# Performance work log

Hardware: AMD Instinct MI355X
Metric: run time of the kernel (lower is better)

The kernel has to match this reference:

```python
import jax, jax.numpy as jnp
import numpy as np

B, T, N, C = 64, 256, 21, 3
HID, HEADS, HDIM, DOUT = 128, 4, 32, 256
CDIM, DMODEL = 64, 256
DINNER, DSTATE, DCONV, DTRANK, L = 512, 16, 4, 16, 4
NSIGNS, NHS, NLOC, NMOV, NORI = 2000, 40, 20, 20, 8
TEMP = 0.07

def _ln(x, w):
    mu = x.mean(-1, keepdims=True)
    var = ((x - mu) ** 2).mean(-1, keepdims=True)
    return (x - mu) / jnp.sqrt(var + 1e-5) * w

def _silu(x):
    return x * jax.nn.sigmoid(x)

def _causal_conv(u, w, b):  # u:(B,T,D), depthwise causal conv, w:(D,K)
    K = w.shape[1]
    up = jnp.pad(u, ((0, 0), (K - 1, 0), (0, 0)))
    y = sum(up[:, k:k + u.shape[1], :] * w[:, k] for k in range(K))
    return y + b

def _scan(u, dt, Bm, Cm, A, Dp):  # selective SSM scan; u,dt:(B,T,Di), Bm,Cm:(B,T,Ds)
    def step(h, xs):
        dt_t, b_t, c_t, u_t = xs
        dA = jnp.exp(dt_t[..., None] * A)                       # (B,Di,Ds)
        dBu = dt_t[..., None] * b_t[:, None, :] * u_t[..., None]
        h = dA * h + dBu
        y = jnp.einsum('bds,bs->bd', h, c_t)
        return h, y
    h0 = jnp.zeros((u.shape[0], A.shape[0], A.shape[1]), u.dtype)
    xs = (dt.swapaxes(0, 1), Bm.swapaxes(0, 1), Cm.swapaxes(0, 1), u.swapaxes(0, 1))
    _, ys = jax.lax.scan(step, h0, xs)
    return ys.swapaxes(0, 1) + u * Dp

def _cos_logits(f, p):
    fn = f / (jnp.linalg.norm(f, axis=-1, keepdims=True) + 1e-8)
    pn = p / (jnp.linalg.norm(p, axis=-1, keepdims=True) + 1e-8)
    return fn @ pn.T / TEMP

def _forward(x, agan_w_in, agan_b_in, agan_w_gat, agan_a_src, agan_a_dst,
             agan_w_out, agan_b_out, pdm_w, pdm_b, pdm_w_fuse, pdm_b_fuse,
             ssm_ln_w, ssm_in_proj, ssm_conv_w, ssm_conv_b, ssm_x_proj,
             ssm_dt_w, ssm_dt_b, ssm_A_log, ssm_D, ssm_out_proj,
             hpc_w_sign, hpc_b_sign, sign_protos, proto_hs, proto_loc,
             proto_mov, proto_ori):
    # ---- AGAN: multi-head graph attention over N landmarks per frame ----
    h0 = jax.nn.relu(x @ agan_w_in + agan_b_in)                  # (B,T,N,HID)
    h = jnp.einsum('btni,hio->btnho', h0, agan_w_gat)            # (B,T,N,H,O)
    src = jnp.einsum('btnho,ho->btnh', h, agan_a_src)
    dst = jnp.einsum('btnho,ho->btnh', h, agan_a_dst)
    e = jax.nn.leaky_relu(src[:, :, :, None, :] + dst[:, :, None, :, :], 0.2)  # (B,T,Ni,Nj,H)
    alpha = jax.nn.softmax(e, axis=3)
    agg = jnp.einsum('btijh,btjho->btiho', alpha, h).reshape(h0.shape)
    feat = jax.nn.relu(h0 + agg)
    spatial = (feat @ agan_w_out + agan_b_out).mean(axis=2)      # (B,T,DOUT)
    # ---- PDM: 4 phonological component projections + fusion ----
    comps = jax.nn.relu(jnp.einsum('btd,kdc->btkc', spatial, pdm_w) + pdm_b)  # (B,T,4,CDIM)
    fused = comps.reshape(B, T, 4 * CDIM) @ pdm_w_fuse + pdm_b_fuse           # (B,T,DMODEL)
    # ---- BiSSM: bidirectional selective SSM layers with residuals ----
    xx = fused
    for l in range(L):
        xn = _ln(xx, ssm_ln_w[l])
        ysum = 0.0
        for d in range(2):
            u_in = xn if d == 0 else xn[:, ::-1]
            xz = u_in @ ssm_in_proj[l, d]
            u, z = xz[..., :DINNER], xz[..., DINNER:]
            u = _silu(_causal_conv(u, ssm_conv_w[l, d], ssm_conv_b[l, d]))
            xdbl = u @ ssm_x_proj[l, d]
            dt = jax.nn.softplus(xdbl[..., :DTRANK] @ ssm_dt_w[l, d] + ssm_dt_b[l, d])
            Bm = xdbl[..., DTRANK:DTRANK + DSTATE]
            Cm = xdbl[..., DTRANK + DSTATE:]
            A = -jnp.exp(ssm_A_log[l, d])
            y = _scan(u, dt, Bm, Cm, A, ssm_D[l, d]) * _silu(z)
            y = y @ ssm_out_proj[l, d]
            ysum = ysum + (y if d == 0 else y[:, ::-1])
        xx = xx + ysum
    temporal = xx
    # ---- HPC: prototype classifier ----
    emb = temporal.mean(axis=1) @ hpc_w_sign + hpc_b_sign        # (B,DMODEL)
    logits = _cos_logits(emb, sign_protos)                       # (B,NSIGNS)
    pooled_c = comps.mean(axis=1)                                # (B,4,CDIM)
    sims = tuple(_cos_logits(pooled_c[:, k], p)
                 for k, p in enumerate((proto_hs, proto_loc, proto_mov, proto_ori)))
    return (logits, emb) + sims

def setup_inputs():
    key = jax.random.key(0)
    ks = iter(jax.random.split(key, 40))
    def rn(shape, scale):
        return jax.random.normal(next(ks), shape, jnp.float32) * scale
    inp = {}
    inp['x'] = rn((B, T, N, C), 1.0)
    inp['agan_w_in'] = rn((C, HID), C ** -0.5)
    inp['agan_b_in'] = jnp.zeros((HID,), jnp.float32)
    inp['agan_w_gat'] = rn((HEADS, HID, HDIM), HID ** -0.5)
    inp['agan_a_src'] = rn((HEADS, HDIM), 0.1)
    inp['agan_a_dst'] = rn((HEADS, HDIM), 0.1)
    inp['agan_w_out'] = rn((HID, DOUT), HID ** -0.5)
    inp['agan_b_out'] = jnp.zeros((DOUT,), jnp.float32)
    inp['pdm_w'] = rn((4, DOUT, CDIM), DOUT ** -0.5)
    inp['pdm_b'] = jnp.zeros((4, CDIM), jnp.float32)
    inp['pdm_w_fuse'] = rn((4 * CDIM, DMODEL), (4 * CDIM) ** -0.5)
    inp['pdm_b_fuse'] = jnp.zeros((DMODEL,), jnp.float32)
    inp['ssm_ln_w'] = jnp.ones((L, DMODEL), jnp.float32)
    inp['ssm_in_proj'] = rn((L, 2, DMODEL, 2 * DINNER), DMODEL ** -0.5)
    inp['ssm_conv_w'] = rn((L, 2, DINNER, DCONV), DCONV ** -0.5)
    inp['ssm_conv_b'] = jnp.zeros((L, 2, DINNER), jnp.float32)
    inp['ssm_x_proj'] = rn((L, 2, DINNER, DTRANK + 2 * DSTATE), DINNER ** -0.5)
    inp['ssm_dt_w'] = rn((L, 2, DTRANK, DINNER), DTRANK ** -0.5)
    inp['ssm_dt_b'] = jnp.full((L, 2, DINNER), -4.6, jnp.float32)  # softplus ~ 0.01
    a = jnp.log(jnp.tile(jnp.arange(1, DSTATE + 1, dtype=jnp.float32)[None, :], (DINNER, 1)))
    inp['ssm_A_log'] = jnp.tile(a[None, None], (L, 2, 1, 1))
    inp['ssm_D'] = jnp.ones((L, 2, DINNER), jnp.float32)
    inp['ssm_out_proj'] = rn((L, 2, DINNER, DMODEL), DINNER ** -0.5)
    inp['hpc_w_sign'] = rn((DMODEL, DMODEL), DMODEL ** -0.5)
    inp['hpc_b_sign'] = jnp.zeros((DMODEL,), jnp.float32)
    inp['sign_protos'] = rn((NSIGNS, DMODEL), 1.0)
    inp['proto_hs'] = rn((NHS, CDIM), 1.0)
    inp['proto_loc'] = rn((NLOC, CDIM), 1.0)
    inp['proto_mov'] = rn((NMOV, CDIM), 1.0)
    inp['proto_ori'] = rn((NORI, CDIM), 1.0)
    return inp

def reference(x, agan_w_in, agan_b_in, agan_w_gat, agan_a_src, agan_a_dst,
              agan_w_out, agan_b_out, pdm_w, pdm_b, pdm_w_fuse, pdm_b_fuse,
              ssm_ln_w, ssm_in_proj, ssm_conv_w, ssm_conv_b, ssm_x_proj,
              ssm_dt_w, ssm_dt_b, ssm_A_log, ssm_D, ssm_out_proj,
              hpc_w_sign, hpc_b_sign, sign_protos, proto_hs, proto_loc,
              proto_mov, proto_ori):
    return _forward(x, agan_w_in, agan_b_in, agan_w_gat, agan_a_src, agan_a_dst,
                    agan_w_out, agan_b_out, pdm_w, pdm_b, pdm_w_fuse, pdm_b_fuse,
                    ssm_ln_w, ssm_in_proj, ssm_conv_w, ssm_conv_b, ssm_x_proj,
                    ssm_dt_w, ssm_dt_b, ssm_A_log, ssm_D, ssm_out_proj,
                    hpc_w_sign, hpc_b_sign, sign_protos, proto_hs, proto_loc,
                    proto_mov, proto_ori)
```

## Files before the change

kernel.cpp:

```cpp
#include <hip/hip_runtime.h>
#include <hip/hip_bf16.h>
#include <math.h>

#define BB 64
#define TT 256
#define NNODE 21
#define HID 128
#define DMODEL 256
#define DINNER 512
#define NSIGNS 2000
#define BTT (BB*TT)

typedef unsigned short u16;
typedef unsigned int u32;
typedef __attribute__((ext_vector_type(8))) short short8;
typedef __attribute__((ext_vector_type(4))) float f32x4;

template<int V> struct IC { static constexpr int v = V; };

__device__ __forceinline__ float siluf(float x){ return x/(1.f+expf(-x)); }
__device__ __forceinline__ u16 f2bf(float x){ __hip_bfloat16 h = __float2bfloat16(x); return *(u16*)&h; }
__device__ __forceinline__ u32 pk2bf(float a, float b){
  float2 f2; f2.x = a; f2.y = b;
  __hip_bfloat162 h2 = __float22bfloat162_rn(f2);
  return *(u32*)&h2;
}
__device__ __forceinline__ float bf2f(u16 u){ return __uint_as_float(((u32)u)<<16); }
__device__ __forceinline__ void gload16(const u16* g, u16* l){
  __builtin_amdgcn_global_load_lds((const __attribute__((address_space(1))) void*)g,
                                   (__attribute__((address_space(3))) void*)l, 16, 0, 0);
}

__global__ __launch_bounds__(256) void transpose_w_kernel(
    const float* __restrict__ in_proj, const float* __restrict__ out_proj,
    const float* __restrict__ x_proj, const float* __restrict__ w_out,
    const float* __restrict__ pdm_w, const float* __restrict__ w_fuse,
    const float* __restrict__ w_gat, u16* __restrict__ dst)
{
  __shared__ short tl[64*66];
  int bx = blockIdx.x, tid = threadIdx.x;
  const float* S = nullptr; size_t soff = 0; int lds = 0, Nsrc = 0;
  size_t doff = 0; int ldd = 0, Nout = 0;
  int tn = 0, tk = 0;
  bool zero = false;
  if (bx < 512) {
    int j = bx >> 5, tt = bx & 31;
    int l = j >> 2, d = j & 1, zh = (j >> 1) & 1;
    tn = tt >> 2; tk = tt & 3;
    S = in_proj; soff = ((size_t)(l*2+d)*256)*1024 + zh*512; lds = 1024; Nsrc = 512;
    doff = (size_t)l*524288 + (size_t)(zh*1024 + d*512)*256; ldd = 256; Nout = 512;
  } else if (bx < 768) {
    int j = (bx-512) >> 5, tt = (bx-512) & 31;
    int l = j >> 1, d = j & 1;
    tn = tt >> 3; tk = tt & 7;
    S = out_proj; soff = (size_t)(l*2+d)*512*256; lds = 256; Nsrc = 256;
    doff = 2097152 + (size_t)l*262144 + d*512; ldd = 1024; Nout = 256;
  } else if (bx < 896) {
    int j = (bx-768) >> 3, tt = (bx-768) & 7;
    int l = j >> 2, sub = j & 3;
    tn = 0; tk = tt;
    if (sub < 2) {
      int d = sub;
      S = x_proj; soff = (size_t)(l*2+d)*512*48; lds = 48; Nsrc = 48;
      doff = 3145728 + (size_t)l*131072 + (size_t)(d*64)*1024 + d*512; ldd = 1024; Nout = 64;
    } else {
      int d = sub-2; zero = true;
      doff = 3145728 + (size_t)l*131072 + (size_t)(d*64)*1024 + (1-d)*512; ldd = 1024; Nout = 64;
    }
  } else if (bx < 904) {
    int tt = bx-896; tn = tt>>1; tk = tt&1;
    S = w_out; soff = 0; lds = 256; Nsrc = 256;
    doff = 3670016; ldd = 128; Nout = 256;
  } else if (bx < 920) {
    int j = (bx-904)>>2, tt = (bx-904)&3;
    tn = 0; tk = tt;
    S = pdm_w; soff = (size_t)j*16384; lds = 64; Nsrc = 64;
    doff = 3702784 + (size_t)j*16384; ldd = 256; Nout = 64;
  } else if (bx < 936) {
    int tt = bx-920; tn = tt>>2; tk = tt&3;
    S = w_fuse; soff = 0; lds = 256; Nsrc = 256;
    doff = 3768320; ldd = 256; Nout = 256;
  } else {
    int j = (bx-936)>>1, tt = (bx-936)&1;
    tn = 0; tk = tt;
    S = w_gat; soff = (size_t)j*4096; lds = 32; Nsrc = 32;
    doff = 3833856 + (size_t)j*4096; ldd = 128; Nout = 32;
  }
  int n0 = tn*64, k0 = tk*64;
  if (!zero) {
    #pragma unroll
    for (int i=0;i<16;++i){
      int kk = i*4 + (tid>>6), nn = tid&63;
      float v = (n0+nn < Nsrc) ? S[soff + (size_t)(k0+kk)*lds + n0+nn] : 0.f;
      tl[nn*66+kk] = (short)f2bf(v);
    }
    __syncthreads();
    #pragma unroll
    for (int i=0;i<16;++i){
      int nn = i*4 + (tid>>6), kk = tid&63;
      if (n0+nn < Nout) dst[doff + (size_t)(n0+nn)*ldd + k0+kk] = (u16)tl[nn*66+kk];
    }
  } else {
    #pragma unroll
    for (int i=0;i<16;++i){
      int nn = i*4 + (tid>>6), kk = tid&63;
      if (n0+nn < Nout) dst[doff + (size_t)(n0+nn)*ldd + k0+kk] = 0;
    }
  }
}

__global__ __launch_bounds__(256) void agan_kernel(
    const float* __restrict__ x, const float* __restrict__ w_in, const float* __restrict__ b_in,
    const u16* __restrict__ bpt, const float* __restrict__ a_src, const float* __restrict__ a_dst,
    u16* __restrict__ fsum_out)
{
  int bt = blockIdx.x;
  int tid = threadIdx.x;
  int lane = tid & 63, wid = tid >> 6;
  int lr = lane & 15, lq = lane >> 4;
  __shared__ float xv[NNODE][4];
  __shared__ __align__(16) short sh0[32*136];
  __shared__ __align__(16) short hmT[128*40];
  __shared__ __align__(16) short alb[4*32*40];
  __shared__ float sd[2][NNODE][4];
  __shared__ float sm[4][NNODE];
  short8 bp[4][2];
  #pragma unroll
  for (int ks=0;ks<4;++ks)
    #pragma unroll
    for (int ct=0;ct<2;++ct)
      bp[ks][ct] = *(const short8*)(bpt + (size_t)(wid*32+ct*16+lr)*128 + ks*32 + lq*8);
  int ii = tid & 127, nn0 = tid >> 7;
  float w0 = w_in[ii], w1 = w_in[128+ii], w2 = w_in[256+ii], bi = b_in[ii];
  if (tid < NNODE*3) xv[tid/3][tid%3] = x[(size_t)bt*63 + tid];
  __syncthreads();
  #pragma unroll
  for (int n = 0; n < 32; n += 2) {
    int nr = n + nn0;
    float v = 0.f;
    if (nr < NNODE)
      v = fmaxf(bi + xv[nr][0]*w0 + xv[nr][1]*w1 + xv[nr][2]*w2, 0.f);
    sh0[nr*136 + ii] = (short)f2bf(v);
  }
  __syncthreads();
  {
    f32x4 g00={},g01={},g10={},g11={};
    #pragma unroll
    for (int ks=0;ks<4;++ks){
      short8 a0 = *(const short8*)&sh0[(lr   )*136 + ks*32 + lq*8];
      short8 a1 = *(const short8*)&sh0[(16+lr)*136 + ks*32 + lq*8];
      g00 = __builtin_amdgcn_mfma_f32_16x16x32_bf16(a0, bp[ks][0], g00, 0,0,0);
      g01 = __builtin_amdgcn_mfma_f32_16x16x32_bf16(a0, bp[ks][1], g01, 0,0,0);
      g10 = __builtin_amdgcn_mfma_f32_16x16x32_bf16(a1, bp[ks][0], g10, 0,0,0);
      g11 = __builtin_amdgcn_mfma_f32_16x16x32_bf16(a1, bp[ks][1], g11, 0,0,0);
    }
    f32x4 gg[2][2] = {{g00,g01},{g10,g11}};
    #pragma unroll
    for (int mt=0;mt<2;++mt)
      #pragma unroll
      for (int ct=0;ct<2;++ct){
        int col = wid*32 + ct*16 + lr;
        int row0 = mt*16 + lq*4;
        u32 wv0 = pk2bf(gg[mt][ct][0], gg[mt][ct][1]);
        u32 wv1 = pk2bf(gg[mt][ct][2], gg[mt][ct][3]);
        *(uint2*)&hmT[col*40 + row0] = make_uint2(wv0,wv1);
      }
  }
  __syncthreads();
  if (tid < 168) {
    int which = tid >= 84;
    int r = tid - which*84;
    int n = r >> 2, h = r & 3;
    const float* av = (which ? a_dst : a_src) + h*32;
    float s = 0.f;
    #pragma unroll
    for (int o=0;o<32;++o){ int oo=(o+tid)&31; s += bf2f((u16)hmT[(h*32+oo)*40 + n])*av[oo]; }
    sd[which][n][h] = s;
  }
  __syncthreads();
  if (tid < 84) {
    int i = tid >> 2, h = tid & 3;
    float sv = sd[0][i][h], m = -1e30f;
    #pragma unroll
    for (int j=0;j<NNODE;++j){
      float e = sv + sd[1][j][h];
      e = e>=0.f ? e : 0.2f*e;
      m = fmaxf(m,e);
    }
    sm[h][i] = m;
  }
  __syncthreads();
  for (int idx = tid; idx < 84*32; idx += 256) {
    int j = idx & 31, ih = idx >> 5;
    int i = ih >> 2, h = ih & 3;
    float m = sm[h][i];
    float ex = 0.f;
    if (j < NNODE){
      float e = sd[0][i][h] + sd[1][j][h];
      e = e>=0.f ? e : 0.2f*e;
      ex = __expf(e - m);
    }
    alb[(h*32+i)*40 + j] = (short)f2bf(ex);
    float s = ex;
    #pragma unroll
    for (int off=1; off<32; off<<=1) s += __shfl_xor(s, off);
    if (j == 0) sm[h][i] = 1.f/s;
  }
  __syncthreads();
  {
    int h = wid;
    short8 a0 = *(const short8*)&alb[(h*32 + lr     )*40 + lq*8];
    short8 a1 = *(const short8*)&alb[(h*32 + 16 + lr)*40 + lq*8];
    short8 b0 = *(const short8*)&hmT[(h*32 + lr     )*40 + lq*8];
    short8 b1 = *(const short8*)&hmT[(h*32 + 16 + lr)*40 + lq*8];
    f32x4 c00={},c01={},c10={},c11={};
    c00 = __builtin_amdgcn_mfma_f32_16x16x32_bf16(a0,b0,c00,0,0,0);
    c01 = __builtin_amdgcn_mfma_f32_16x16x32_bf16(a0,b1,c01,0,0,0);
    c10 = __builtin_amdgcn_mfma_f32_16x16x32_bf16(a1,b0,c10,0,0,0);
    c11 = __builtin_amdgcn_mfma_f32_16x16x32_bf16(a1,b1,c11,0,0,0);
    f32x4 cc[2][2] = {{c00,c01},{c10,c11}};
    #pragma unroll
    for (int ct=0; ct<2; ++ct){
      int col = h*32 + ct*16 + lr;
      float s = 0.f;
      #pragma unroll
      for (int mt=0; mt<2; ++mt)
        #pragma unroll
        for (int r=0;r<4;++r){
          int n = mt*16 + lq*4 + r;
          if (n < NNODE)
            s += fmaxf(bf2f((u16)sh0[n*136+col]) + cc[mt][ct][r]*sm[h][n], 0.f);
        }
      s += __shfl_xor(s, 16);
      s += __shfl_xor(s, 32);
      if (lq == 0) fsum_out[(size_t)bt*128 + col] = f2bf(s*(1.f/21.f));
    }
  }
}

template<int ACC, int BIAS, int RELU, int SM>
__global__ __launch_bounds__(256) void gemm_bf16_kernel(
    const u16* __restrict__ A, const u16* __restrict__ BT, const float* __restrict__ bias,
    float* __restrict__ C, u16* __restrict__ C2,
    int M, int N, int K, int lda)
{
  __shared__ __align__(16) short Asl[8192];
  __shared__ __align__(16) short Bsl[8192];
  int tid = threadIdx.x;
  int lane = tid & 63, wid = tid >> 6;
  int wm = wid >> 1, wn = wid & 1;
  int row0 = blockIdx.y*128, col0 = blockIdx.x*128;
  const u16* Ab = A  + (size_t)row0*lda;
  const u16* Bb = BT + (size_t)col0*K;
  f32x4 acc[4][4] = {};
  int lrow = lane & 15, lk = (lane>>4)*8;
  for (int k0 = 0; k0 < K; k0 += 64) {
    #pragma unroll
    for (int is=0; is<4; ++is){
      int li = is*256 + tid;
      int row = li >> 3;
      int c8  = (li & 7) ^ (row & 7);
      gload16(Ab + (size_t)row*lda + k0 + c8*8, (u16*)Asl + ((is<<8)+(wid<<6))*8);
      gload16(Bb + (size_t)row*K   + k0 + c8*8, (u16*)Bsl + ((is<<8)+(wid<<6))*8);
    }
    __syncthreads();
    #pragma unroll
    for (int ksub=0; ksub<2; ++ksub){
      int slot = (ksub*32 + lk) >> 3;
      short8 a[4], b[4];
      #pragma unroll
      for (int i=0;i<4;++i){ int rr=wm*64+i*16+lrow; a[i]=*(const short8*)&Asl[rr*64+((slot^(rr&7))<<3)]; }
      #pragma unroll
      for (int j=0;j<4;++j){ int rr=wn*64+j*16+lrow; b[j]=*(const short8*)&Bsl[rr*64+((slot^(rr&7))<<3)]; }
      #pragma unroll
      for (int i=0;i<4;++i)
        #pragma unroll
        for (int j=0;j<4;++j)
          acc[i][j] = __builtin_amdgcn_mfma_f32_16x16x32_bf16(a[i], b[j], acc[i][j], 0, 0, 0);
    }
    __syncthreads();
  }
  #pragma unroll
  for (int i=0;i<4;++i) {
    int row = row0 + wm*64 + i*16 + (lane>>4)*4;
    #pragma unroll
    for (int j=0;j<4;++j) {
      int col = col0 + wn*64 + j*16 + (lane&15);
      if (col < N) {
        float bv = BIAS ? bias[col] : 0.f;
        #pragma unroll
        for (int r=0;r<4;++r) {
          float v = acc[i][j][r] + bv;
          if (RELU) v = fmaxf(v, 0.f);
          size_t o = (size_t)(row+r)*N + col;
          if (ACC)           C[o] += v;
          else if (SM == 0)  C[o]  = v;
          else               C2[o] = f2bf(v);
        }
      }
    }
  }
}

template<int ACC, int BIAS, int RELU, int SM, int POOL>
__global__ __launch_bounds__(256) void gemm_bm64_kernel(
    const u16* __restrict__ A, const u16* __restrict__ BT, const float* __restrict__ bias,
    float* __restrict__ C, u16* __restrict__ C2, float* __restrict__ pool,
    int M, int N, int K, int lda)
{
  __shared__ __align__(16) short Asl[4096];
  __shared__ __align__(16) short Bsl[8192];
  int tid = threadIdx.x;
  int lane = tid & 63, wid = tid >> 6;
  int wm = wid >> 1, wn = wid & 1;
  int row0 = blockIdx.y*64, col0 = blockIdx.x*128;
  const u16* Ab = A  + (size_t)row0*lda;
  const u16* Bb = BT + (size_t)col0*K;
  f32x4 acc[2][4] = {};
  int lrow = lane & 15, lq = lane >> 4, lk = lq*8;
  for (int k0 = 0; k0 < K; k0 += 64) {
    #pragma unroll
    for (int is=0; is<2; ++is){
      int li = is*256 + tid;
      int row = li >> 3;
      int c8  = (li & 7) ^ (row & 7);
      gload16(Ab + (size_t)row*lda + k0 + c8*8, (u16*)Asl + ((is<<8)+(wid<<6))*8);
    }
    #pragma unroll
    for (int is=0; is<4; ++is){
      int li = is*256 + tid;
      int row = li >> 3;
      int c8  = (li & 7) ^ (row & 7);
      gload16(Bb + (size_t)row*K + k0 + c8*8, (u16*)Bsl + ((is<<8)+(wid<<6))*8);
    }
    __syncthreads();
    #pragma unroll
    for (int ksub=0; ksub<2; ++ksub){
      int slot = (ksub*32 + lk) >> 3;
      short8 a[2], b[4];
      #pragma unroll
      for (int i=0;i<2;++i){ int rr=wm*32+i*16+lrow; a[i]=*(const short8*)&Asl[rr*64+((slot^(rr&7))<<3)]; }
      #pragma unroll
      for (int j=0;j<4;++j){ int rr=wn*64+j*16+lrow; b[j]=*(const short8*)&Bsl[rr*64+((slot^(rr&7))<<3)]; }
      #pragma unroll
      for (int i=0;i<2;++i)
        #pragma unroll
        for (int j=0;j<4;++j)
          acc[i][j] = __builtin_amdgcn_mfma_f32_16x16x32_bf16(a[i], b[j], acc[i][j], 0, 0, 0);
    }
    __syncthreads();
  }
  float colsum[4] = {0.f,0.f,0.f,0.f};
  #pragma unroll
  for (int i=0;i<2;++i) {
    int row = row0 + wm*32 + i*16 + lq*4;
    #pragma unroll
    for (int j=0;j<4;++j) {
      int col = col0 + wn*64 + j*16 + lrow;
      if (col < N) {
        float bv = BIAS ? bias[col] : 0.f;
        #pragma unroll
        for (int r=0;r<4;++r) {
          float v = acc[i][j][r] + bv;
          if (RELU) v = fmaxf(v, 0.f);
          size_t o = (size_t)(row+r)*N + col;
          if (ACC)           C[o] += v;
          else if (SM == 0)  C[o]  = v;
          else               C2[o] = f2bf(v);
          if (POOL) colsum[j] += v;
        }
      }
    }
  }
  if (POOL) {
    float* red = (float*)Asl;
    #pragma unroll
    for (int j=0;j<4;++j) red[tid*4+j] = colsum[j];
    __syncthreads();
    if (tid < 128) {
      int wn_ = tid >> 6, j_ = (tid >> 4) & 3, l15 = tid & 15;
      float s = 0.f;
      #pragma unroll
      for (int wm_=0;wm_<2;++wm_)
        #pragma unroll
        for (int g=0;g<4;++g)
          s += red[(((wm_*2+wn_)*64) + g*16 + l15)*4 + j_];
      pool[(size_t)blockIdx.y*256 + blockIdx.x*128 + tid] = s * (1.f/256.f);
    }
  }
}

__global__ __launch_bounds__(256) void gemm_n64_kernel(
    const u16* __restrict__ A, const u16* __restrict__ BT,
    float* __restrict__ C, int N, int K, int lda)
{
  __shared__ __align__(16) short Asl[4096];
  __shared__ __align__(16) short Bsl[4096];
  int tid = threadIdx.x;
  int lane = tid & 63, wid = tid >> 6;
  int lrow = lane & 15, lq = lane >> 4, lk = lq*8;
  int row0 = blockIdx.y*64, col0 = blockIdx.x*64;
  const u16* Ab = A  + (size_t)row0*lda;
  const u16* Bb = BT + (size_t)col0*K;
  f32x4 acc[4] = {};
  for (int k0 = 0; k0 < K; k0 += 64) {
    #pragma unroll
    for (int is=0; is<2; ++is){
      int li = is*256 + tid;
      int row = li >> 3;
      int c8  = (li & 7) ^ (row & 7);
      gload16(Ab + (size_t)row*lda + k0 + c8*8, (u16*)Asl + ((is<<8)+(wid<<6))*8);
      gload16(Bb + (size_t)row*K   + k0 + c8*8, (u16*)Bsl + ((is<<8)+(wid<<6))*8);
    }
    __syncthreads();
    #pragma unroll
    for (int ksub=0; ksub<2; ++ksub){
      int slot = (ksub*32 + lk) >> 3;
      int arr = wid*16 + lrow;
      short8 av = *(const short8*)&Asl[arr*64 + ((slot^(arr&7))<<3)];
      #pragma unroll
      for (int j=0;j<4;++j){
        int brr = j*16 + lrow;
        short8 bv = *(const short8*)&Bsl[brr*64 + ((slot^(brr&7))<<3)];
        acc[j] = __builtin_amdgcn_mfma_f32_16x16x32_bf16(av, bv, acc[j], 0, 0, 0);
      }
    }
    __syncthreads();
  }
  #pragma unroll
  for (int j=0;j<4;++j){
    int col = col0 + j*16 + lrow;
    #pragma unroll
    for (int r=0;r<4;++r){
      int row = row0 + wid*16 + lq*4 + r;
      C[(size_t)row*N + col] = acc[j][r];
    }
  }
}

__global__ __launch_bounds__(256) void ln_kernel(const float* __restrict__ x,
    const float* __restrict__ w, u16* __restrict__ o)
{
  int row = blockIdx.x*4 + (threadIdx.x>>6);
  int lane = threadIdx.x & 63;
  float4 v = *(const float4*)(x + (size_t)row*DMODEL + lane*4);
  float s = v.x+v.y+v.z+v.w;
  #pragma unroll
  for (int off=32;off>=1;off>>=1) s += __shfl_xor(s, off);
  float mu = s * (1.f/256.f);
  float d0=v.x-mu, d1=v.y-mu, d2=v.z-mu, d3=v.w-mu;
  float q = d0*d0+d1*d1+d2*d2+d3*d3;
  #pragma unroll
  for (int off=32;off>=1;off>>=1) q += __shfl_xor(q, off);
  float inv = 1.f/sqrtf(q*(1.f/256.f) + 1e-5f);
  float4 wv = *(const float4*)(w + lane*4);
  uint2 pk; pk.x = pk2bf(d0*inv*wv.x, d1*inv*wv.y); pk.y = pk2bf(d2*inv*wv.z, d3*inv*wv.w);
  *(uint2*)(o + (size_t)row*DMODEL + lane*4) = pk;
}

__global__ __launch_bounds__(256) void conv_kernel(const u16* __restrict__ xz,
    const float* __restrict__ cw, const float* __restrict__ cb,
    u16* __restrict__ ucv)
{
  int idx = blockIdx.x*256 + threadIdx.x;
  int du8 = idx & 127, dir = du8 >> 6, d8 = (du8 & 63) << 3;
  int bt = idx >> 7, t = bt & 255;
  const u16* up = xz + (size_t)(bt - t)*2048 + dir*512 + d8;
  float w[8][4];
  #pragma unroll
  for (int j=0;j<8;++j){
    float4 wv = *(const float4*)(cw + (size_t)dir*2048 + (d8+j)*4);
    w[j][0]=wv.x; w[j][1]=wv.y; w[j][2]=wv.z; w[j][3]=wv.w;
  }
  float s[8];
  float4 cb0 = *(const float4*)(cb + dir*512 + d8);
  float4 cb1 = *(const float4*)(cb + dir*512 + d8 + 4);
  s[0]=cb0.x; s[1]=cb0.y; s[2]=cb0.z; s[3]=cb0.w;
  s[4]=cb1.x; s[5]=cb1.y; s[6]=cb1.z; s[7]=cb1.w;
  if (dir == 0) {
    #pragma unroll
    for (int k=0;k<4;++k){
      int tk = t-3+k;
      if (tk >= 0){
        short8 uv = *(const short8*)(up + (size_t)tk*2048);
        #pragma unroll
        for (int j=0;j<8;++j) s[j] += w[j][k]*bf2f((u16)uv[j]);
      }
    }
  } else {
    #pragma unroll
    for (int kk=0;kk<4;++kk){
      int tk = t+kk;
      if (tk < TT){
        short8 uv = *(const short8*)(up + (size_t)tk*2048);
        #pragma unroll
        for (int j=0;j<8;++j) s[j] += w[j][3-kk]*bf2f((u16)uv[j]);
      }
    }
  }
  short8 o;
  #pragma unroll
  for (int j=0;j<8;++j) o[j] = (short)f2bf(siluf(s[j]));
  *(short8*)(ucv + (size_t)bt*1024 + dir*512 + d8) = o;
}

template<int FINAL>
__global__ __launch_bounds__(256) void scan_phase_kernel(
    const u16* __restrict__ ucv, const float* __restrict__ xd, const u16* __restrict__ xz,
    const float* __restrict__ dtw, const float* __restrict__ dtb,
    const float* __restrict__ alog, const float* __restrict__ dvec,
    const u16* __restrict__ hend_r, const float* __restrict__ sdt_r,
    float* __restrict__ sdt_w, u16* __restrict__ hend_w,
    u16* __restrict__ yout)
{
  int b = blockIdx.x, c = blockIdx.y, gz = blockIdx.z;
  int d = gz >> 1;
  int tid = threadIdx.x;
  int dd = ((gz & 1) << 8) + tid;
  float wdt[16], Av[16], h[16];
  #pragma unroll
  for (int s=0;s<16;++s){
    wdt[s] = dtw[d*8192 + s*512 + dd];
    Av[s]  = -__expf(alog[d*8192 + dd*16 + s]);
    h[s]   = 0.f;
  }
  float bdt = dtb[d*512 + dd];
  bool powok = true;
  #pragma unroll
  for (int s=0;s<16;++s) powok = powok && (fabsf(Av[s] + (float)(s+1)) < 1e-5f*(float)(s+1));
  __shared__ float sxd[32][48];
  for (int i = tid; i < 1536; i += 256){
    int q = i/48, r = i - q*48;
    int p = (c<<5)+q, t = d ? 255-p : p;
    sxd[q][r] = xd[((size_t)b*TT + t)*128 + d*64 + r];
  }
  if (FINAL) {
    for (int cp=0; cp<c; ++cp){
      size_t cbase = (((size_t)b*8+cp)*2+d)*512 + dd;
      float S = sdt_r[cbase];
      short8 h0v = *(const short8*)(hend_r + cbase*16);
      short8 h1v = *(const short8*)(hend_r + cbase*16 + 8);
      #pragma unroll
      for (int s=0;s<8;++s)  h[s]   = fmaf(__expf(Av[s]*S),   h[s],   bf2f((u16)h0v[s]));
      #pragma unroll
      for (int s=0;s<8;++s)  h[s+8] = fmaf(__expf(Av[s+8]*S), h[s+8], bf2f((u16)h1v[s]));
    }
  }
  __syncthreads();
  float S = 0.f;
  float Dv = FINAL ? dvec[d*512 + dd] : 0.f;
  const u16* ub = ucv + d*512 + dd;
  const u16* zb = xz + 1024 + d*512 + dd;
  u16* yb = yout + d*512 + dd;
  auto qloop = [&](auto icpow){
    constexpr int POW = decltype(icpow)::v;
    #pragma unroll 4
    for (int q=0;q<32;++q) {
      int p = (c<<5)+q, t = d ? 255-p : p;
      size_t row = (size_t)b*TT + t;
      float uc = bf2f(ub[row*1024]);
      float zc = FINAL ? bf2f(zb[row*2048]) : 0.f;
      const float* sr = sxd[q];
      float p0=0.f,p1=0.f,p2=0.f,p3=0.f;
      #pragma unroll
      for (int r=0;r<16;r+=4){
        p0 = fmaf(sr[r+0],wdt[r+0],p0);
        p1 = fmaf(sr[r+1],wdt[r+1],p1);
        p2 = fmaf(sr[r+2],wdt[r+2],p2);
        p3 = fmaf(sr[r+3],wdt[r+3],p3);
      }
      float dtp = bdt + ((p0+p1)+(p2+p3));
      float dt = fmaxf(dtp,0.f) + __logf(1.f + __expf(-fabsf(dtp)));
      float dtu = dt*uc;
      if (!FINAL) S += dt;
      float y0=0.f, y1=0.f;
      if (POW) {
        float rr = __expf(-dt);
        float pw = rr;
        #pragma unroll
        for (int s=0;s<16;++s){
          h[s] = fmaf(pw, h[s], dtu*sr[16+s]);
          if (FINAL) y0 = fmaf(h[s], sr[32+s], y0);
          pw *= rr;
        }
      } else {
        #pragma unroll
        for (int s=0;s<16;s+=2){
          float dA0 = __expf(dt*Av[s]);
          float dA1 = __expf(dt*Av[s+1]);
          h[s]   = fmaf(dA0, h[s],   dtu*sr[16+s]);
          h[s+1] = fmaf(dA1, h[s+1], dtu*sr[16+s+1]);
          if (FINAL){ y0 = fmaf(h[s],sr[32+s],y0); y1 = fmaf(h[s+1],sr[32+s+1],y1); }
        }
      }
      if (FINAL){
        float yv = (y0+y1) + uc*Dv;
        float sg = zc / (1.f + __expf(-zc));
        yb[row*2048] = f2bf(yv*sg);
      }
    }
  };
  if (powok) qloop(IC<1>{}); else qloop(IC<0>{});
  if (!FINAL){
    size_t co = (((size_t)b*8+c)*2+d)*512 + dd;
    sdt_w[co] = S;
    short8 o0, o1;
    #pragma unroll
    for (int s=0;s<8;++s){ o0[s] = (short)f2bf(h[s]); o1[s] = (short)f2bf(h[s+8]); }
    *(short8*)(hend_w + co*16)     = o0;
    *(short8*)(hend_w + co*16 + 8) = o1;
  }
}

__global__ __launch_bounds__(256) void emb_kernel(const float* __restrict__ xx,
    const float* __restrict__ wsgn, const float* __restrict__ bsgn,
    float* __restrict__ embw, float* __restrict__ out)
{
  int b = blockIdx.x, tid = threadIdx.x;
  __shared__ float mt[256];
  float s0=0.f,s1=0.f,s2=0.f,s3=0.f;
  for (int t=0;t<TT;t+=4){
    s0 += xx[((size_t)b*TT+t  )*DMODEL + tid];
    s1 += xx[((size_t)b*TT+t+1)*DMODEL + tid];
    s2 += xx[((size_t)b*TT+t+2)*DMODEL + tid];
    s3 += xx[((size_t)b*TT+t+3)*DMODEL + tid];
  }
  mt[tid] = (s0+s1+s2+s3)*(1.f/256.f);
  __syncthreads();
  float acc = bsgn[tid];
  for (int i=0;i<DMODEL;++i) acc += mt[i]*wsgn[i*DMODEL + tid];
  embw[b*DMODEL+tid] = acc;
  out[128000 + b*DMODEL + tid] = acc;
}

__global__ __launch_bounds__(256) void head_kernel(const float* __restrict__ embw,
    const float* __restrict__ protos, const float* __restrict__ part,
    const float* __restrict__ phs, const float* __restrict__ ploc,
    const float* __restrict__ pmov, const float* __restrict__ pori,
    float* __restrict__ out)
{
  int b = blockIdx.x, qt = blockIdx.y, tid = threadIdx.x;
  __shared__ __align__(16) float e[256];
  __shared__ float red[4];
  if (qt == 4) {
    e[tid] = part[(size_t)(4*b)*256 + tid] + part[(size_t)(4*b+1)*256 + tid]
           + part[(size_t)(4*b+2)*256 + tid] + part[(size_t)(4*b+3)*256 + tid];
    __syncthreads();
    if (tid < 4) {
      float ss = 0.f;
      for (int i=0;i<64;++i){ float q = e[tid*64+i]; ss += q*q; }
      red[tid] = 1.f/(sqrtf(ss)+1e-8f);
    }
    __syncthreads();
    if (tid < 88) {
      int k, pi; const float* P; size_t off; int npk;
      if (tid < 40)      { k=0; pi=tid;    P=phs;  off=144384; npk=40; }
      else if (tid < 60) { k=1; pi=tid-40; P=ploc; off=146944; npk=20; }
      else if (tid < 80) { k=2; pi=tid-60; P=pmov; off=148224; npk=20; }
      else               { k=3; pi=tid-80; P=pori; off=149504; npk=8;  }
      float dot=0.f, ps=0.f;
      for (int i=0;i<64;++i){ float pv = P[pi*64+i]; dot += pv*e[k*64+i]; ps += pv*pv; }
      out[off + (size_t)b*npk + pi] = dot*red[k]/(sqrtf(ps)+1e-8f)*(1.f/0.07f);
    }
    return;
  }
  float acc = embw[b*DMODEL + tid];
  e[tid] = acc;
  __syncthreads();
  float v = acc*acc;
  #pragma unroll
  for (int off=32;off>=1;off>>=1) v += __shfl_xor(v, off);
  if ((tid&63)==0) red[tid>>6] = v;
  __syncthreads();
  float esc = 1.f/(sqrtf(red[0]+red[1]+red[2]+red[3]) + 1e-8f);
  int pend = qt*500 + 500;
  for (int p = qt*500 + tid; p < pend; p += 256) {
    const float* pr = protos + (size_t)p*256;
    float dot=0.f, ps=0.f;
    for (int i=0;i<256;i+=4) {
      float4 pv = *(const float4*)(pr+i);
      float4 ev = *(const float4*)(e+i);
      dot += pv.x*ev.x + pv.y*ev.y + pv.z*ev.z + pv.w*ev.w;
      ps  += pv.x*pv.x + pv.y*pv.y + pv.z*pv.z + pv.w*pv.w;
    }
    out[(size_t)b*NSIGNS + p] = dot*esc/(sqrtf(ps)+1e-8f)*(1.f/0.07f);
  }
}

extern "C" void kernel_launch(void* const* d_in, const int* in_sizes, int n_in,
                              void* d_out, int out_size, void* d_ws, size_t ws_size,
                              hipStream_t stream) {
  const float* x         = (const float*)d_in[0];
  const float* w_in      = (const float*)d_in[1];
  const float* b_in      = (const float*)d_in[2];
  const float* w_gat     = (const float*)d_in[3];
  const float* a_src     = (const float*)d_in[4];
  const float* a_dst     = (const float*)d_in[5];
  const float* w_out     = (const float*)d_in[6];
  const float* b_out     = (const float*)d_in[7];
  const float* pdm_w     = (const float*)d_in[8];
  const float* pdm_b     = (const float*)d_in[9];
  const float* w_fuse    = (const float*)d_in[10];
  const float* b_fuse    = (const float*)d_in[11];
  const float* ln_w      = (const float*)d_in[12];
  const float* in_proj   = (const float*)d_in[13];
  const float* conv_w    = (const float*)d_in[14];
  const float* conv_b    = (const float*)d_in[15];
  const float* x_proj    = (const float*)d_in[16];
  const float* dt_w      = (const float*)d_in[17];
  const float* dt_b      = (const float*)d_in[18];
  const float* A_log     = (const float*)d_in[19];
  const float* Dvec      = (const float*)d_in[20];
  const float* out_proj  = (const float*)d_in[21];
  const float* w_sign    = (const float*)d_in[22];
  const float* b_sign    = (const float*)d_in[23];
  const float* protos    = (const float*)d_in[24];
  const float* phs       = (const float*)d_in[25];
  const float* ploc      = (const float*)d_in[26];
  const float* pmov      = (const float*)d_in[27];
  const float* pori      = (const float*)d_in[28];
  float* out = (float*)d_out;

  float* wsf = (float*)d_ws;
  const size_t f_xx    = 0;
  const size_t f_xdbl  = f_xx   + 4194304;
  const size_t f_part  = f_xdbl + 2097152;
  const size_t f_emb   = f_part + 65536;
  const size_t f_end   = f_emb  + 16384;
  u16* wsu = (u16*)(wsf + f_end);
  const size_t u_xn    = 0;
  const size_t u_xz    = u_xn   + 4194304;
  const size_t u_ucv   = u_xz   + 33554432;
  const size_t u_fsum  = u_ucv  + 16777216;
  const size_t u_spat  = u_fsum + 2097152;
  const size_t u_comps = u_spat + 4194304;
  const size_t u_w     = u_comps+ 4194304;
  u16* wiT = wsu + u_w;
  u16* woT = wiT + 2097152;
  u16* wxT = woT + 1048576;
  u16* wA  = wxT + 524288;
  u16* wB  = wA  + 32768;
  u16* wF  = wB  + 65536;
  u16* wBp = wF  + 65536;
  u16*   hstate = wsu + u_fsum;
  float* sdt    = (float*)(wsu + u_fsum + 8388608);

  transpose_w_kernel<<<944, 256, 0, stream>>>(in_proj, out_proj, x_proj, w_out, pdm_w, w_fuse, w_gat, wsu + u_w);
  agan_kernel<<<BTT, 256, 0, stream>>>(x, w_in, b_in, wBp, a_src, a_dst, wsu + u_fsum);
  gemm_bm64_kernel<0,1,0,1,0><<<dim3(2,256), 256, 0, stream>>>(wsu+u_fsum, wA, b_out, nullptr, wsu+u_spat, nullptr, BTT, 256, 128, 128);
  gemm_bm64_kernel<0,1,1,1,1><<<dim3(2,256), 256, 0, stream>>>(wsu+u_spat, wB, pdm_b, nullptr, wsu+u_comps, wsf+f_part, BTT, 256, 256, 256);
  gemm_bm64_kernel<0,1,0,0,0><<<dim3(2,256), 256, 0, stream>>>(wsu+u_comps, wF, b_fuse, wsf+f_xx, nullptr, nullptr, BTT, 256, 256, 256);

  for (int l = 0; l < 4; ++l) {
    ln_kernel<<<BTT/4, 256, 0, stream>>>(wsf+f_xx, ln_w + l*DMODEL, wsu+u_xn);
    gemm_bf16_kernel<0,0,0,1><<<dim3(16,128), 256, 0, stream>>>(wsu+u_xn, wiT + (size_t)l*524288,
        nullptr, nullptr, wsu+u_xz, BTT, 2048, 256, 256);
    conv_kernel<<<BTT*128/256, 256, 0, stream>>>(wsu+u_xz, conv_w + (size_t)l*4096,
        conv_b + (size_t)l*1024, wsu+u_ucv);
    gemm_n64_kernel<<<dim3(2,256), 256, 0, stream>>>(wsu+u_ucv, wxT + (size_t)l*131072,
        wsf+f_xdbl, 128, 1024, 1024);
    scan_phase_kernel<0><<<dim3(64,7,4), 256, 0, stream>>>(wsu+u_ucv, wsf+f_xdbl, nullptr,
        dt_w + (size_t)l*16384, dt_b + (size_t)l*1024,
        A_log + (size_t)l*16384, nullptr,
        nullptr, nullptr, sdt, hstate, nullptr);
    scan_phase_kernel<1><<<dim3(64,8,4), 256, 0, stream>>>(wsu+u_ucv, wsf+f_xdbl, wsu+u_xz,
        dt_w + (size_t)l*16384, dt_b + (size_t)l*1024,
        A_log + (size_t)l*16384, Dvec + (size_t)l*1024,
        hstate, sdt, nullptr, nullptr, wsu+u_xz);
    gemm_bm64_kernel<1,0,0,0,0><<<dim3(2,256), 256, 0, stream>>>(wsu+u_xz, woT + (size_t)l*262144,
        nullptr, wsf+f_xx, nullptr, nullptr, BTT, 256, 1024, 2048);
  }

  emb_kernel<<<64, 256, 0, stream>>>(wsf+f_xx, w_sign, b_sign, wsf+f_emb, out);
  head_kernel<<<dim3(64,5), 256, 0, stream>>>(wsf+f_emb, protos, wsf+f_part, phs, ploc, pmov, pori, out);
  (void)in_sizes; (void)n_in; (void)out_size; (void)ws_size;
}
```

Before: 1.151 ms.

## Fold attention vectors into GAT weights and trim scan-phase loads and exps

Precomputes w_gat·a_src and w_gat·a_dst as a small bf16 matrix in the weight-transpose kernel. The AGAN kernel then gets the src/dst attention scores from two extra MFMAs on wave 0, replacing a separate LDS dot-product pass and one barrier. The scan phase kernel loads only the 32 columns it needs in the non-final pass. When A follows the -(s+1) pattern, the final pass builds the chunk-carry decay factors from powers of one exp instead of 16 exps. Scores now come from bf16 h0 against bf16 folded weights rather than from the bf16-rounded h, which slightly changes rounding.

After: 1.142 ms (median of 2 runs). Within noise of the previous version (-0.8%).

```diff
diff --git a/kernel.cpp b/kernel.cpp
--- a/kernel.cpp
+++ b/kernel.cpp
@@ -35,10 +35,26 @@
     const float* __restrict__ in_proj, const float* __restrict__ out_proj,
     const float* __restrict__ x_proj, const float* __restrict__ w_out,
     const float* __restrict__ pdm_w, const float* __restrict__ w_fuse,
-    const float* __restrict__ w_gat, u16* __restrict__ dst)
+    const float* __restrict__ w_gat, const float* __restrict__ a_src,
+    const float* __restrict__ a_dst, u16* __restrict__ dst)
 {
   __shared__ short tl[64*66];
   int bx = blockIdx.x, tid = threadIdx.x;
+  if (bx == 944) {
+    for (int j = tid; j < 2048; j += 256) {
+      int c = j >> 7, i = j & 127;
+      float v = 0.f;
+      if (c < 8) {
+        int which = c >> 2, h = c & 3;
+        const float* a = (which ? a_dst : a_src) + h*32;
+        const float* wg = w_gat + (size_t)h*4096 + i*32;
+        #pragma unroll
+        for (int o=0;o<32;++o) v += wg[o]*a[o];
+      }
+      dst[3850240 + j] = f2bf(v);
+    }
+    return;
+  }
   const float* S = nullptr; size_t soff = 0; int lds = 0, Nsrc = 0;
   size_t doff = 0; int ldd = 0, Nout = 0;
   int tn = 0, tk = 0;
@@ -111,7 +127,7 @@
 
 __global__ __launch_bounds__(256) void agan_kernel(
     const float* __restrict__ x, const float* __restrict__ w_in, const float* __restrict__ b_in,
-    const u16* __restrict__ bpt, const float* __restrict__ a_src, const float* __restrict__ a_dst,
+    const u16* __restrict__ bpt, const u16* __restrict__ wsd,
     u16* __restrict__ fsum_out)
 {
   int bt = blockIdx.x;
@@ -144,7 +160,7 @@
   }
   __syncthreads();
   {
-    f32x4 g00={},g01={},g10={},g11={};
+    f32x4 g00={},g01={},g10={},g11={},s0v={},s1v={};
     #pragma unroll
     for (int ks=0;ks<4;++ks){
       short8 a0 = *(const short8*)&sh0[(lr   )*136 + ks*32 + lq*8];
@@ -153,6 +169,11 @@
       g01 = __builtin_amdgcn_mfma_f32_16x16x32_bf16(a0, bp[ks][1], g01, 0,0,0);
       g10 = __builtin_amdgcn_mfma_f32_16x16x32_bf16(a1, bp[ks][0], g10, 0,0,0);
       g11 = __builtin_amdgcn_mfma_f32_16x16x32_bf16(a1, bp[ks][1], g11, 0,0,0);
+      if (wid == 0) {
+        short8 wb = *(const short8*)(wsd + (size_t)lr*128 + ks*32 + lq*8);
+        s0v = __builtin_amdgcn_mfma_f32_16x16x32_bf16(a0, wb, s0v, 0,0,0);
+        s1v = __builtin_amdgcn_mfma_f32_16x16x32_bf16(a1, wb, s1v, 0,0,0);
+      }
     }
     f32x4 gg[2][2] = {{g00,g01},{g10,g11}};
     #pragma unroll
@@ -165,17 +186,15 @@
         u32 wv1 = pk2bf(gg[mt][ct][2], gg[mt][ct][3]);
         *(uint2*)&hmT[col*40 + row0] = make_uint2(wv0,wv1);
       }
-  }
-  __syncthreads();
-  if (tid < 168) {
-    int which = tid >= 84;
-    int r = tid - which*84;
-    int n = r >> 2, h = r & 3;
-    const float* av = (which ? a_dst : a_src) + h*32;
-    float s = 0.f;
-    #pragma unroll
-    for (int o=0;o<32;++o){ int oo=(o+tid)&31; s += bf2f((u16)hmT[(h*32+oo)*40 + n])*av[oo]; }
-    sd[which][n][h] = s;
+    if (wid == 0 && lr < 8) {
+      int which = lr >> 2, h = lr & 3;
+      #pragma unroll
+      for (int r=0;r<4;++r){
+        int n0_ = lq*4 + r, n1_ = 16 + lq*4 + r;
+        if (n0_ < NNODE) sd[which][n0_][h] = s0v[r];
+        if (n1_ < NNODE) sd[which][n1_][h] = s1v[r];
+      }
+    }
   }
   __syncthreads();
   if (tid < 84) {
@@ -529,21 +548,44 @@
   #pragma unroll
   for (int s=0;s<16;++s) powok = powok && (fabsf(Av[s] + (float)(s+1)) < 1e-5f*(float)(s+1));
   __shared__ float sxd[32][48];
-  for (int i = tid; i < 1536; i += 256){
-    int q = i/48, r = i - q*48;
-    int p = (c<<5)+q, t = d ? 255-p : p;
-    sxd[q][r] = xd[((size_t)b*TT + t)*128 + d*64 + r];
-  }
   if (FINAL) {
-    for (int cp=0; cp<c; ++cp){
-      size_t cbase = (((size_t)b*8+cp)*2+d)*512 + dd;
-      float S = sdt_r[cbase];
-      short8 h0v = *(const short8*)(hend_r + cbase*16);
-      short8 h1v = *(const short8*)(hend_r + cbase*16 + 8);
-      #pragma unroll
-      for (int s=0;s<8;++s)  h[s]   = fmaf(__expf(Av[s]*S),   h[s],   bf2f((u16)h0v[s]));
-      #pragma unroll
-      for (int s=0;s<8;++s)  h[s+8] = fmaf(__expf(Av[s+8]*S), h[s+8], bf2f((u16)h1v[s]));
+    for (int i = tid; i < 1536; i += 256){
+      int q = i/48, r = i - q*48;
+      int p = (c<<5)+q, t = d ? 255-p : p;
+      sxd[q][r] = xd[((size_t)b*TT + t)*128 + d*64 + r];
+    }
+  } else {
+    for (int i = tid; i < 1024; i += 256){
+      int q = i>>5, r = i&31;
+      int p = (c<<5)+q, t = d ? 255-p : p;
+      sxd[q][r] = xd[((size_t)b*TT + t)*128 + d*64 + r];
+    }
+  }
+  if (FINAL) {
+    if (powok) {
+      for (int cp=0; cp<c; ++cp){
+        size_t cbase = (((size_t)b*8+cp)*2+d)*512 + dd;
+        float S = sdt_r[cbase];
+        float e1 = __expf(-S);
+        short8 h0v = *(const short8*)(hend_r + cbase*16);
+        short8 h1v = *(const short8*)(hend_r + cbase*16 + 8);
+        float pw = e1;
+        #pragma unroll
+        for (int s=0;s<8;++s){ h[s] = fmaf(pw, h[s], bf2f((u16)h0v[s])); pw *= e1; }
+        #pragma unroll
+        for (int s=0;s<8;++s){ h[s+8] = fmaf(pw, h[s+8], bf2f((u16)h1v[s])); pw *= e1; }
+      }
+    } else {
+      for (int cp=0; cp<c; ++cp){
+        size_t cbase = (((size_t)b*8+cp)*2+d)*512 + dd;
+        float S = sdt_r[cbase];
+        short8 h0v = *(const short8*)(hend_r + cbase*16);
+        short8 h1v = *(const short8*)(hend_r + cbase*16 + 8);
+        #pragma unroll
+        for (int s=0;s<8;++s)  h[s]   = fmaf(__expf(Av[s]*S),   h[s],   bf2f((u16)h0v[s]));
+        #pragma unroll
+        for (int s=0;s<8;++s)  h[s+8] = fmaf(__expf(Av[s+8]*S), h[s+8], bf2f((u16)h1v[s]));
+      }
     }
   }
   __syncthreads();
@@ -742,11 +784,12 @@
   u16* wB  = wA  + 32768;
   u16* wF  = wB  + 65536;
   u16* wBp = wF  + 65536;
+  u16* wSd = wBp + 16384;
   u16*   hstate = wsu + u_fsum;
   float* sdt    = (float*)(wsu + u_fsum + 8388608);
 
-  transpose_w_kernel<<<944, 256, 0, stream>>>(in_proj, out_proj, x_proj, w_out, pdm_w, w_fuse, w_gat, wsu + u_w);
-  agan_kernel<<<BTT, 256, 0, stream>>>(x, w_in, b_in, wBp, a_src, a_dst, wsu + u_fsum);
+  transpose_w_kernel<<<945, 256, 0, stream>>>(in_proj, out_proj, x_proj, w_out, pdm_w, w_fuse, w_gat, a_src, a_dst, wsu + u_w);
+  agan_kernel<<<BTT, 256, 0, stream>>>(x, w_in, b_in, wBp, wSd, wsu + u_fsum);
   gemm_bm64_kernel<0,1,0,1,0><<<dim3(2,256), 256, 0, stream>>>(wsu+u_fsum, wA, b_out, nullptr, wsu+u_spat, nullptr, BTT, 256, 128, 128);
   gemm_bm64_kernel<0,1,1,1,1><<<dim3(2,256), 256, 0, stream>>>(wsu+u_spat, wB, pdm_b, nullptr, wsu+u_comps, wsf+f_part, BTT, 256, 256, 256);
   gemm_bm64_kernel<0,1,0,0,0><<<dim3(2,256), 256, 0, stream>>>(wsu+u_comps, wF, b_fuse, wsf+f_xx, nullptr, nullptr, BTT, 256, 256, 256);
```
